# Kernel tuning notes

Measured on AMD Instinct MI355X. Metric: run time of the kernel, lower is better.

The kernel has to match this reference:

```python
import jax, jax.numpy as jnp
import numpy as np

# constants from source: INTERNAL_DIM=768, NUM_MEMORY_NETWORKS=8, NUM_SUB_NETWORKS=2, NUM_LAYERS=2
T, B, D, M, S, L, H = 8, 32, 768, 8, 2, 2, 8
d = D // S  # 384, per-subnetwork hidden dim
EPS = 1e-5


def _ln(x, g, b):
    mu = x.mean(-1, keepdims=True)
    v = ((x - mu) ** 2).mean(-1, keepdims=True)
    return (x - mu) / jnp.sqrt(v + EPS) * g + b


def setup_inputs() -> dict:
    key = jax.random.key(0)
    ks = jax.random.split(key, 10)
    rn = lambda k, shape, s: jax.random.normal(k, shape, jnp.float32) * s
    return {
        'x': rn(ks[0], (T, B, D), 1.0),
        'mem0': rn(ks[1], (M, B, D), 0.02),
        'attn_in_w': rn(ks[2], (M, 3 * D, D), D ** -0.5),
        'attn_in_b': jnp.zeros((M, 3 * D), jnp.float32),
        'attn_out_w': rn(ks[3], (M, D, D), D ** -0.5),
        'attn_out_b': jnp.zeros((M, D), jnp.float32),
        'heb_w': rn(ks[4], (M, S, L, d, d), 0.01),
        'heb_rw': rn(ks[5], (M, S, L, d, d), 0.01),
        'alpha': jnp.full((M, S, L, d), 0.02, jnp.float32),
        'decay': jnp.full((M, S, L, d), 0.005, jnp.float32),
        'ln_act_g': jnp.ones((M, S, L, d), jnp.float32),
        'ln_act_b': jnp.zeros((M, S, L, d), jnp.float32),
        'ln_rec_g': jnp.ones((M, S, L, d), jnp.float32),
        'ln_rec_b': jnp.zeros((M, S, L, d), jnp.float32),
        'pred_w1': rn(ks[6], (M, S, L, d, d), d ** -0.5),
        'pred_b1': jnp.zeros((M, S, L, d), jnp.float32),
        'pred_w2': rn(ks[7], (M, S, L, d, 3 * d), d ** -0.5),
        'pred_b2': jnp.zeros((M, S, L, 3 * d), jnp.float32),
        'out_w': rn(ks[8], (M, D, D), D ** -0.5),
        'out_b': jnp.zeros((M, D), jnp.float32),
        'ln_out_g': jnp.ones((M, D), jnp.float32),
        'ln_out_b': jnp.zeros((M, D), jnp.float32),
    }


def _mha(q, kv, in_w, in_b, out_w, out_b):
    # torch nn.MultiheadAttention: q [B,D], kv [Mkv,B,D] (seq-first)
    wq, wk, wv = in_w[:D], in_w[D:2 * D], in_w[2 * D:]
    bq, bk, bv = in_b[:D], in_b[D:2 * D], in_b[2 * D:]
    hd = D // H
    qh = (q @ wq.T + bq).reshape(B, H, hd) * hd ** -0.5
    kh = (kv @ wk.T + bk).reshape(-1, B, H, hd)
    vh = (kv @ wv.T + bv).reshape(-1, B, H, hd)
    a = jax.nn.softmax(jnp.einsum('bhd,sbhd->bhs', qh, kh), axis=-1)
    o = jnp.einsum('bhs,sbhd->bhd', a, vh).reshape(B, D)
    return o @ out_w.T + out_b


def _heb(xin, pa, pr, dp, sr, gb, W, Wr, W0, Wr0, al, dc, lag, lab, lrg, lrb, w1, b1, w2, b2):
    # one HebbianLayer step; xin/pa/pr/... [B,d], W/Wr [d,d]
    sg = jax.lax.stop_gradient
    # update_neuromodulators (previous neuromodulator state is detached in torch)
    nt = (jax.nn.relu(pa @ w1 + b1) @ w2 + b2).reshape(B, d, 3)
    pd, ps, pg = nt[..., 0], nt[..., 1], nt[..., 2]
    inv = 1.0 / jnp.maximum(ps, 1e-6)  # clamp(min=1e-6)
    dp = jnp.tanh(dp + pd * inv)
    sr = jax.nn.sigmoid(sr + ps)
    gb = jax.nn.sigmoid(gb + pg * inv)
    # hebbian_update: torch writes via .data.copy_ -> fully non-differentiable
    mod = al[None] * dp * sr  # [B,d] modulated alpha

    def upd(prev, Wm):
        a_sm = jax.nn.softmax(prev, axis=1)
        w_sm = jax.nn.softmax(Wm, axis=1)
        # mean_b a_sm[b,i] * mod[b,j] * w_sm[i,j]  (no [B,d,d] intermediate)
        return w_sm * (jnp.einsum('bi,bj->ij', a_sm, mod) / B)

    sd = dc * jax.nn.sigmoid(gb.mean(axis=0))  # scaled decay, diag
    W_new = sg(W + upd(pa, W) - sd[:, None] * W)
    Wr_new = sg(Wr + upd(pr, Wr) - sd[:, None] * Wr)
    # forward matmul uses the updated weight VALUE, gradient accumulates on leaf param
    W_eff = W_new + W0 - sg(W0)
    Wr_eff = Wr_new + Wr0 - sg(Wr0)
    rec = _ln(pa @ Wr_eff, lrg, lrb)
    act = _ln(jax.nn.relu(xin @ W_eff + rec), lag, lab)
    return act, (sg(act), sg(rec), sg(dp), sg(sr), sg(gb), W_new, Wr_new)


_heb_vm = jax.vmap(_heb)  # over P = M*S parallel subnetwork-layers


def reference(x, mem0, attn_in_w, attn_in_b, attn_out_w, attn_out_b, heb_w, heb_rw,
              alpha, decay, ln_act_g, ln_act_b, ln_rec_g, ln_rec_b,
              pred_w1, pred_b1, pred_w2, pred_b2, out_w, out_b, ln_out_g, ln_out_b):
    P = M * S
    rs = lambda a: a.reshape((P, L) + a.shape[3:])
    hw, hrw = rs(heb_w), rs(heb_rw)
    al, dc = rs(alpha), rs(decay)
    lag, lab, lrg, lrb = rs(ln_act_g), rs(ln_act_b), rs(ln_rec_g), rs(ln_rec_b)
    w1, b1, w2, b2 = rs(pred_w1), rs(pred_b1), rs(pred_w2), rs(pred_b2)
    z = jnp.zeros((P, L, B, d), x.dtype)
    carry0 = (mem0, z, z, z, z, z, hw, hrw)

    def step(carry, x_t):
        mem, pa, pr, dp, sr, gb, Wst, Wrst = carry
        # attention message passing: each memory network attends over all memories
        attn = jax.vmap(_mha, in_axes=(None, None, 0, 0, 0, 0))(
            x_t, mem, attn_in_w, attn_in_b, attn_out_w, attn_out_b)  # [M,B,D]
        # split into subnetworks: chunk i = u[:, i*d:(i+1)*d]
        h = attn.reshape(M, B, S, d).transpose(0, 2, 1, 3).reshape(P, B, d)
        new_st = []
        for l in range(L):
            h, st = _heb_vm(h, pa[:, l], pr[:, l], dp[:, l], sr[:, l], gb[:, l],
                            Wst[:, l], Wrst[:, l], hw[:, l], hrw[:, l],
                            al[:, l], dc[:, l], lag[:, l], lab[:, l], lrg[:, l], lrb[:, l],
                            w1[:, l], b1[:, l], w2[:, l], b2[:, l])
            new_st.append(st)
        stacked = tuple(jnp.stack([new_st[l][i] for l in range(L)], axis=1) for i in range(7))
        cat = h.reshape(M, S, B, d).transpose(0, 2, 1, 3).reshape(M, B, D)
        out = jnp.einsum('mbd,med->mbe', cat, out_w) + out_b[:, None]
        out = _ln(out, ln_out_g[:, None], ln_out_b[:, None])  # [M,B,D]
        return (out,) + stacked, out

    carry, _ = jax.lax.scan(step, carry0, x)
    return carry[0]  # final memory activations [M,B,D]
```

## Files before the change

kernel.cpp:

```cpp
#include <hip/hip_runtime.h>
#include <math.h>

namespace {

constexpr int T_ = 8, B_ = 32, D_ = 768, M_ = 8, S_ = 2, L_ = 2, H_ = 8;
constexpr int d_ = D_ / S_;
constexpr int P_ = M_ * S_;
constexpr int HD = D_ / H_;
constexpr float EPSF = 1e-5f;
constexpr int KNOFOLD = 1 << 30;

__device__ __forceinline__ float wredS(float v) {
#pragma unroll
  for (int o = 32; o; o >>= 1) v += __shfl_xor(v, o);
  return v;
}
__device__ __forceinline__ float wredM(float v) {
#pragma unroll
  for (int o = 32; o; o >>= 1) v = fmaxf(v, __shfl_xor(v, o));
  return v;
}
__device__ __forceinline__ float blockSum(float v, float* red, int nw) {
  v = wredS(v);
  if ((threadIdx.x & 63) == 0) red[threadIdx.x >> 6] = v;
  __syncthreads();
  float r = 0.f;
  for (int i = 0; i < nw; ++i) r += red[i];
  __syncthreads();
  return r;
}
__device__ __forceinline__ float blockMax(float v, float* red, int nw) {
  v = wredM(v);
  if ((threadIdx.x & 63) == 0) red[threadIdx.x >> 6] = v;
  __syncthreads();
  float r = red[0];
  for (int i = 1; i < nw; ++i) r = fmaxf(r, red[i]);
  __syncthreads();
  return r;
}
__device__ __forceinline__ float sigm(float x) { return 1.f / (1.f + expf(-x)); }

template <bool TRANSB, int EPI>
__device__ __forceinline__ void gemm_body(
    const float* __restrict__ Ab, int lda, const float* __restrict__ Wb,
    const float* __restrict__ biasz, float* __restrict__ Cb, int r0, int n0,
    int N, int K, float scale, int kfold, int kfoldOff) {
  __shared__ float As[32][36];
  __shared__ float Bs[32][132];
  const int tid = threadIdx.x;
  const int rg = tid >> 4, cg = tid & 15;
  float acc[2][8];
#pragma unroll
  for (int i = 0; i < 2; ++i)
#pragma unroll
    for (int j = 0; j < 8; ++j) acc[i][j] = 0.f;
  for (int k0 = 0; k0 < K; k0 += 32) {
    const float* Ak = Ab + (k0 >= kfold ? kfoldOff : 0);
    const int k0e = k0 - (k0 >= kfold ? kfold : 0);
    {
      const int r = tid >> 3, kq = (tid & 7) << 2;
      const float4 v = *(const float4*)(Ak + (size_t)(r0 + r) * lda + k0e + kq);
      As[kq + 0][r] = v.x; As[kq + 1][r] = v.y;
      As[kq + 2][r] = v.z; As[kq + 3][r] = v.w;
    }
#pragma unroll
    for (int i = 0; i < 4; ++i) {
      const int li = tid + i * 256;
      if (TRANSB) {
        const int n = li >> 3, kq = (li & 7) << 2;
        const float4 v = *(const float4*)(Wb + (size_t)(n0 + n) * K + k0 + kq);
        Bs[kq + 0][n] = v.x; Bs[kq + 1][n] = v.y;
        Bs[kq + 2][n] = v.z; Bs[kq + 3][n] = v.w;
      } else {
        const int k = li >> 5, nq = (li & 31) << 2;
        const float4 v = *(const float4*)(Wb + (size_t)(k0 + k) * N + n0 + nq);
        *(float4*)&Bs[k][nq] = v;
      }
    }
    __syncthreads();
#pragma unroll
    for (int kk = 0; kk < 32; ++kk) {
      const float2 a = *(const float2*)&As[kk][rg * 2];
      const float4 b0 = *(const float4*)&Bs[kk][cg * 4];
      const float4 b1 = *(const float4*)&Bs[kk][cg * 4 + 64];
      acc[0][0] += a.x * b0.x; acc[0][1] += a.x * b0.y;
      acc[0][2] += a.x * b0.z; acc[0][3] += a.x * b0.w;
      acc[0][4] += a.x * b1.x; acc[0][5] += a.x * b1.y;
      acc[0][6] += a.x * b1.z; acc[0][7] += a.x * b1.w;
      acc[1][0] += a.y * b0.x; acc[1][1] += a.y * b0.y;
      acc[1][2] += a.y * b0.z; acc[1][3] += a.y * b0.w;
      acc[1][4] += a.y * b1.x; acc[1][5] += a.y * b1.y;
      acc[1][6] += a.y * b1.z; acc[1][7] += a.y * b1.w;
    }
    __syncthreads();
  }
  float bv[8] = {0.f, 0.f, 0.f, 0.f, 0.f, 0.f, 0.f, 0.f};
  if (biasz) {
    const float* bb = biasz + n0 + cg * 4;
#pragma unroll
    for (int j = 0; j < 4; ++j) { bv[j] = bb[j]; bv[4 + j] = bb[64 + j]; }
  }
#pragma unroll
  for (int i = 0; i < 2; ++i) {
#pragma unroll
    for (int half = 0; half < 2; ++half) {
      float4 o;
      o.x = acc[i][half * 4 + 0] + bv[half * 4 + 0];
      o.y = acc[i][half * 4 + 1] + bv[half * 4 + 1];
      o.z = acc[i][half * 4 + 2] + bv[half * 4 + 2];
      o.w = acc[i][half * 4 + 3] + bv[half * 4 + 3];
      if (EPI == 1) {
        o.x = fmaxf(o.x, 0.f); o.y = fmaxf(o.y, 0.f);
        o.z = fmaxf(o.z, 0.f); o.w = fmaxf(o.w, 0.f);
      }
      if (EPI == 2) { o.x *= scale; o.y *= scale; o.z *= scale; o.w *= scale; }
      *(float4*)(Cb + (size_t)(r0 + rg * 2 + i) * N + n0 + half * 64 + cg * 4) = o;
    }
  }
}

template <bool TRANSB, int EPI>
__global__ __launch_bounds__(256) void k_gemm(
    const float* __restrict__ A, int sAhi, int sAlo, int lda,
    const float* __restrict__ W, int sW, const float* __restrict__ bias, int sB,
    float* __restrict__ C, int sC, int N, int K, float scale, int kfold,
    int kfoldOff) {
  const int z = blockIdx.z;
  const float* Ab = A + (size_t)(z >> 1) * sAhi + (size_t)(z & 1) * sAlo;
  const float* Wb = W + (size_t)z * sW;
  const float* biasz = bias ? bias + (size_t)z * sB : nullptr;
  float* Cb = C + (size_t)z * sC;
  gemm_body<TRANSB, EPI>(Ab, lda, Wb, biasz, Cb, blockIdx.y * 32,
                         blockIdx.x * 128, N, K, scale, kfold, kfoldOff);
}

__global__ __launch_bounds__(256) void k_recact(
    const float* __restrict__ A0, int hi0, int lo0, int lda0,
    const float* __restrict__ W0,
    const float* __restrict__ A1, int hi1, int lo1, int lda1,
    const float* __restrict__ W1, int sW, float* __restrict__ C0,
    float* __restrict__ C1) {
  const int z = blockIdx.z;
  const int which = z >> 4, zz = z & 15;
  const float* Ab = which ? A1 + (size_t)(zz >> 1) * hi1 + (size_t)(zz & 1) * lo1
                          : A0 + (size_t)(zz >> 1) * hi0 + (size_t)(zz & 1) * lo0;
  const int lda = which ? lda1 : lda0;
  const float* Wb = (which ? W1 : W0) + (size_t)zz * sW;
  float* Cb = (which ? C1 : C0) + (size_t)zz * (B_ * d_);
  gemm_body<false, 0>(Ab, lda, Wb, nullptr, Cb, 0, blockIdx.x * 128, d_, d_,
                      1.f, KNOFOLD, 0);
}

__global__ __launch_bounds__(64) void k_attn(const float* __restrict__ qb,
    const float* __restrict__ kvb, float* __restrict__ ob) {
  __shared__ float as_[8][8];
  const int mb = blockIdx.x, m = mb >> 5, b = mb & 31;
  const int t = threadIdx.x, h = t >> 3, s = t & 7;
  const float* qrow = qb + (size_t)mb * D_ + h * HD;
  const float* krow = kvb + ((size_t)m * 256 + s * 32 + b) * (2 * D_) + h * HD;
  float sc = 0.f;
#pragma unroll 8
  for (int e = 0; e < HD; ++e) sc += qrow[e] * krow[e];
  float mx = sc;
#pragma unroll
  for (int o = 1; o < 8; o <<= 1) mx = fmaxf(mx, __shfl_xor(mx, o));
  const float ex = expf(sc - mx);
  float sm = ex;
#pragma unroll
  for (int o = 1; o < 8; o <<= 1) sm += __shfl_xor(sm, o);
  as_[h][s] = ex / sm;
  __syncthreads();
  const float* vbase = kvb + (size_t)m * 256 * (2 * D_) + D_;
  for (int e = t; e < D_; e += 64) {
    const int hh = e / HD;
    float o = 0.f;
#pragma unroll
    for (int ss = 0; ss < 8; ++ss)
      o += as_[hh][ss] * vbase[(size_t)(ss * 32 + b) * (2 * D_) + e];
    ob[(size_t)mb * D_ + e] = o;
  }
}

__global__ __launch_bounds__(384) void k_mod(const float* __restrict__ nt,
    float* __restrict__ dp, float* __restrict__ sr, float* __restrict__ gb,
    float* __restrict__ mod, float* __restrict__ sd,
    const float* __restrict__ alpha, const float* __restrict__ decay, int l) {
  const int p = blockIdx.x, j = threadIdx.x;
  const int pl = p * L_ + l;
  const float al = alpha[(size_t)pl * d_ + j];
  const float dc = decay[(size_t)pl * d_ + j];
  const size_t sbase = (size_t)pl * B_ * d_;
  float gsum = 0.f;
  for (int b = 0; b < B_; ++b) {
    const float* row = nt + ((size_t)p * B_ + b) * (3 * d_) + 3 * j;
    const float pd = row[0], ps = row[1], pg = row[2];
    const float inv = 1.f / fmaxf(ps, 1e-6f);
    const size_t ix = sbase + (size_t)b * d_ + j;
    const float dpv = tanhf(dp[ix] + pd * inv);
    const float srv = sigm(sr[ix] + ps);
    const float gbv = sigm(gb[ix] + pg * inv);
    dp[ix] = dpv; sr[ix] = srv; gb[ix] = gbv;
    mod[((size_t)p * B_ + b) * d_ + j] = al * dpv * srv;
    gsum += gbv;
  }
  sd[(size_t)p * d_ + j] = dc * sigm(gsum * (1.f / B_));
}

__global__ __launch_bounds__(256) void k_wsm(float* __restrict__ Wst,
    float* __restrict__ Wrst, const float* __restrict__ pa,
    const float* __restrict__ pr, const float* __restrict__ mod,
    const float* __restrict__ sd, int l) {
  __shared__ float mods[B_][d_];
  __shared__ float asms[8][B_];
  __shared__ float rm_s[B_], rs_s[B_];
  __shared__ float red[4];
  const int i0 = blockIdx.x * 8, p = blockIdx.y, which = blockIdx.z;
  const int tid = threadIdx.x;
  const int pl = p * L_ + l;
  float* W = (which ? Wrst : Wst) + (size_t)pl * d_ * d_;
  const float* act = (which ? pr : pa) + (size_t)pl * B_ * d_;
  for (int ix = tid; ix < B_ * d_; ix += 256)
    mods[ix / d_][ix % d_] = mod[(size_t)p * B_ * d_ + ix];
  {
    const int bb = tid >> 3, l8 = tid & 7;
    const float* ar = act + (size_t)bb * d_;
    float mx = -3.4e38f;
    for (int j = l8; j < d_; j += 8) mx = fmaxf(mx, ar[j]);
#pragma unroll
    for (int o = 1; o < 8; o <<= 1) mx = fmaxf(mx, __shfl_xor(mx, o));
    float s = 0.f;
    for (int j = l8; j < d_; j += 8) s += expf(ar[j] - mx);
#pragma unroll
    for (int o = 1; o < 8; o <<= 1) s += __shfl_xor(s, o);
    if (l8 == 0) { rm_s[bb] = mx; rs_s[bb] = s; }
  }
  __syncthreads();
  {
    const int ii = tid >> 5, b = tid & 31;
    asms[ii][b] = expf(act[(size_t)b * d_ + i0 + ii] - rm_s[b]) / rs_s[b];
  }
  __syncthreads();
  for (int ii = 0; ii < 8; ++ii) {
    const int i = i0 + ii;
    float* Wrow = W + (size_t)i * d_;
    const float w1v = Wrow[tid];
    const bool a2 = tid < (d_ - 256);
    const float w2v = a2 ? Wrow[tid + 256] : 0.f;
    const float mx = blockMax(a2 ? fmaxf(w1v, w2v) : w1v, red, 4);
    const float e1 = expf(w1v - mx);
    const float e2 = a2 ? expf(w2v - mx) : 0.f;
    const float ssum = blockSum(e1 + e2, red, 4);
    const float sdi = sd[(size_t)p * d_ + i];
    float o1 = 0.f, o2 = 0.f;
    const float* am = asms[ii];
#pragma unroll 8
    for (int b = 0; b < B_; ++b) {
      const float a = am[b];
      o1 += a * mods[b][tid];
      if (a2) o2 += a * mods[b][tid + 256];
    }
    Wrow[tid] = w1v * (1.f - sdi) + (e1 / ssum) * (o1 * (1.f / B_));
    if (a2) Wrow[tid + 256] = w2v * (1.f - sdi) + (e2 / ssum) * (o2 * (1.f / B_));
    __syncthreads();
  }
}

__global__ __launch_bounds__(128) void k_lnpair(const float* __restrict__ gr,
    const float* __restrict__ ga, float* __restrict__ prs,
    float* __restrict__ pas, const float* __restrict__ lrg,
    const float* __restrict__ lrb, const float* __restrict__ lag,
    const float* __restrict__ lab, int l) {
  __shared__ float red[2];
  const int pb = blockIdx.x, p = pb >> 5, b = pb & 31;
  const int pl = p * L_ + l;
  const int t = threadIdx.x;
  const size_t soff = ((size_t)pl * B_ + b) * d_;
  const float* xr = gr + (size_t)pb * d_;
  float v0 = xr[t], v1 = xr[t + 128], v2 = xr[t + 256];
  float mu = blockSum(v0 + v1 + v2, red, 2) * (1.f / d_);
  float e0 = v0 - mu, e1 = v1 - mu, e2 = v2 - mu;
  float va = blockSum(e0 * e0 + e1 * e1 + e2 * e2, red, 2) * (1.f / d_);
  float inv = 1.f / sqrtf(va + EPSF);
  const float* G = lrg + (size_t)pl * d_;
  const float* Bv = lrb + (size_t)pl * d_;
  const float r0v = e0 * inv * G[t] + Bv[t];
  const float r1v = e1 * inv * G[t + 128] + Bv[t + 128];
  const float r2v = e2 * inv * G[t + 256] + Bv[t + 256];
  prs[soff + t] = r0v;
  prs[soff + t + 128] = r1v;
  prs[soff + t + 256] = r2v;
  const float* xa = ga + (size_t)pb * d_;
  float a0 = fmaxf(xa[t] + r0v, 0.f);
  float a1 = fmaxf(xa[t + 128] + r1v, 0.f);
  float a2 = fmaxf(xa[t + 256] + r2v, 0.f);
  mu = blockSum(a0 + a1 + a2, red, 2) * (1.f / d_);
  e0 = a0 - mu; e1 = a1 - mu; e2 = a2 - mu;
  va = blockSum(e0 * e0 + e1 * e1 + e2 * e2, red, 2) * (1.f / d_);
  inv = 1.f / sqrtf(va + EPSF);
  const float* G2 = lag + (size_t)pl * d_;
  const float* B2 = lab + (size_t)pl * d_;
  pas[soff + t] = e0 * inv * G2[t] + B2[t];
  pas[soff + t + 128] = e1 * inv * G2[t + 128] + B2[t + 128];
  pas[soff + t + 256] = e2 * inv * G2[t + 256] + B2[t + 256];
}

__global__ __launch_bounds__(256) void k_lnout(const float* __restrict__ pre,
    float* __restrict__ memo, const float* __restrict__ gg,
    const float* __restrict__ bb) {
  __shared__ float red[4];
  const int mb = blockIdx.x, m = mb >> 5;
  const float* x = pre + (size_t)mb * D_;
  const int t = threadIdx.x;
  const float v0 = x[t], v1 = x[t + 256], v2 = x[t + 512];
  const float mu = blockSum(v0 + v1 + v2, red, 4) * (1.f / D_);
  const float e0 = v0 - mu, e1 = v1 - mu, e2 = v2 - mu;
  const float va = blockSum(e0 * e0 + e1 * e1 + e2 * e2, red, 4) * (1.f / D_);
  const float inv = 1.f / sqrtf(va + EPSF);
  const float* G = gg + (size_t)m * D_;
  const float* Bv = bb + (size_t)m * D_;
  float* o = memo + (size_t)mb * D_;
  o[t] = e0 * inv * G[t] + Bv[t];
  o[t + 256] = e1 * inv * G[t + 256] + Bv[t + 256];
  o[t + 512] = e2 * inv * G[t + 512] + Bv[t + 512];
}

}

extern "C" void kernel_launch(void* const* d_in, const int* in_sizes, int n_in,
                              void* d_out, int out_size, void* d_ws, size_t ws_size,
                              hipStream_t stream) {
  const float* x     = (const float*)d_in[0];
  const float* mem0  = (const float*)d_in[1];
  const float* ainw  = (const float*)d_in[2];
  const float* ainb  = (const float*)d_in[3];
  const float* aoutw = (const float*)d_in[4];
  const float* aoutb = (const float*)d_in[5];
  const float* hebw  = (const float*)d_in[6];
  const float* hebrw = (const float*)d_in[7];
  const float* alpha = (const float*)d_in[8];
  const float* decay = (const float*)d_in[9];
  const float* lag   = (const float*)d_in[10];
  const float* lab   = (const float*)d_in[11];
  const float* lrg   = (const float*)d_in[12];
  const float* lrb   = (const float*)d_in[13];
  const float* pw1   = (const float*)d_in[14];
  const float* pb1   = (const float*)d_in[15];
  const float* pw2   = (const float*)d_in[16];
  const float* pb2   = (const float*)d_in[17];
  const float* outw  = (const float*)d_in[18];
  const float* outb  = (const float*)d_in[19];
  const float* lng   = (const float*)d_in[20];
  const float* lnb   = (const float*)d_in[21];

  float* w = (float*)d_ws;
  size_t off = 0;
  auto alloc = [&](size_t n) { float* p = w + off; off += n; return p; };
  float* mem   = alloc((size_t)M_ * B_ * D_);
  float* qb    = alloc((size_t)M_ * B_ * D_);
  float* kvb   = alloc((size_t)M_ * M_ * B_ * 2 * D_);
  float* ob    = alloc((size_t)M_ * B_ * D_);
  float* attnh = alloc((size_t)M_ * B_ * D_);
  float* t1    = alloc((size_t)P_ * B_ * d_);
  float* nt    = alloc((size_t)P_ * B_ * 3 * d_);
  float* modb  = alloc((size_t)P_ * B_ * d_);
  float* sdb   = alloc((size_t)P_ * d_);
  float* gtmp  = alloc((size_t)2 * P_ * B_ * d_);
  float* otmp  = alloc((size_t)M_ * B_ * D_);
  float* pa    = alloc((size_t)P_ * L_ * B_ * d_);
  float* pr    = alloc((size_t)P_ * L_ * B_ * d_);
  float* dp    = alloc((size_t)P_ * L_ * B_ * d_);
  float* sr    = alloc((size_t)P_ * L_ * B_ * d_);
  float* gbst  = alloc((size_t)P_ * L_ * B_ * d_);
  float* Wst   = alloc((size_t)P_ * L_ * d_ * d_);
  float* Wrst  = alloc((size_t)P_ * L_ * d_ * d_);
  float* gtmp0 = gtmp;
  float* gtmp1 = gtmp + (size_t)P_ * B_ * d_;
  (void)in_sizes; (void)n_in; (void)out_size; (void)ws_size;

  hipMemcpyAsync(mem, mem0, sizeof(float) * M_ * B_ * D_, hipMemcpyDeviceToDevice, stream);
  hipMemcpyAsync(Wst, hebw, sizeof(float) * P_ * L_ * d_ * d_, hipMemcpyDeviceToDevice, stream);
  hipMemcpyAsync(Wrst, hebrw, sizeof(float) * P_ * L_ * d_ * d_, hipMemcpyDeviceToDevice, stream);
  hipMemsetAsync(pa, 0, sizeof(float) * 5 * P_ * L_ * B_ * d_, stream);

  const float qscale = 1.0f / sqrtf((float)HD);
  const int LBd = L_ * B_ * d_;
  const int Bd = B_ * d_;

  auto gemm = [&](bool transB, int epi, const float* A, int sAhi, int sAlo,
                  int lda, const float* Wp, int sW, const float* bias, int sB,
                  float* C, int sC, int R, int N, int K, int G, float scale,
                  int kfold, int kfoldOff) {
    dim3 grid(N / 128, R / 32, G), blk(256);
    if (transB && epi == 0)
      k_gemm<true, 0><<<grid, blk, 0, stream>>>(A, sAhi, sAlo, lda, Wp, sW, bias, sB, C, sC, N, K, scale, kfold, kfoldOff);
    else if (transB && epi == 2)
      k_gemm<true, 2><<<grid, blk, 0, stream>>>(A, sAhi, sAlo, lda, Wp, sW, bias, sB, C, sC, N, K, scale, kfold, kfoldOff);
    else if (!transB && epi == 0)
      k_gemm<false, 0><<<grid, blk, 0, stream>>>(A, sAhi, sAlo, lda, Wp, sW, bias, sB, C, sC, N, K, scale, kfold, kfoldOff);
    else
      k_gemm<false, 1><<<grid, blk, 0, stream>>>(A, sAhi, sAlo, lda, Wp, sW, bias, sB, C, sC, N, K, scale, kfold, kfoldOff);
  };

  for (int t = 0; t < T_; ++t) {
    const float* xt = x + (size_t)t * B_ * D_;
    gemm(true, 2, xt, 0, 0, D_, ainw, 3 * D_ * D_, ainb, 3 * D_, qb, B_ * D_,
         B_, D_, D_, M_, qscale, KNOFOLD, 0);
    gemm(true, 0, mem, 0, 0, D_, ainw + D_ * D_, 3 * D_ * D_, ainb + D_, 3 * D_,
         kvb, M_ * B_ * 2 * D_, M_ * B_, 2 * D_, D_, M_, 1.f, KNOFOLD, 0);
    k_attn<<<dim3(M_ * B_), dim3(64), 0, stream>>>(qb, kvb, ob);
    gemm(true, 0, ob, 2 * B_ * D_, B_ * D_, D_, aoutw, D_ * D_, aoutb, D_,
         attnh, B_ * D_, B_, D_, D_, M_, 1.f, KNOFOLD, 0);

    for (int l = 0; l < L_; ++l) {
      gemm(false, 1, pa + (size_t)l * Bd, 2 * LBd, LBd, d_,
           pw1 + (size_t)l * d_ * d_, L_ * d_ * d_, pb1 + l * d_, L_ * d_,
           t1, Bd, B_, d_, d_, P_, 1.f, KNOFOLD, 0);
      gemm(false, 0, t1, 2 * Bd, Bd, d_, pw2 + (size_t)l * d_ * 3 * d_,
           L_ * d_ * 3 * d_, pb2 + l * 3 * d_, L_ * 3 * d_, nt, 3 * Bd,
           B_, 3 * d_, d_, P_, 1.f, KNOFOLD, 0);
      k_mod<<<dim3(P_), dim3(d_), 0, stream>>>(nt, dp, sr, gbst, modb, sdb,
                                               alpha, decay, l);
      k_wsm<<<dim3(d_ / 8, P_, 2), dim3(256), 0, stream>>>(Wst, Wrst, pa, pr,
                                                           modb, sdb, l);
      if (l == 0)
        k_recact<<<dim3(3, 1, 32), dim3(256), 0, stream>>>(
            pa + (size_t)l * Bd, 2 * LBd, LBd, d_, Wrst + (size_t)l * d_ * d_,
            attnh, B_ * D_, d_, D_, Wst + (size_t)l * d_ * d_,
            L_ * d_ * d_, gtmp0, gtmp1);
      else
        k_recact<<<dim3(3, 1, 32), dim3(256), 0, stream>>>(
            pa + (size_t)l * Bd, 2 * LBd, LBd, d_, Wrst + (size_t)l * d_ * d_,
            pa, 2 * LBd, LBd, d_, Wst + (size_t)l * d_ * d_,
            L_ * d_ * d_, gtmp0, gtmp1);
      k_lnpair<<<dim3(P_ * B_), dim3(128), 0, stream>>>(gtmp0, gtmp1, pr, pa,
                                                        lrg, lrb, lag, lab, l);
    }

    gemm(true, 0, pa + Bd, 8 * Bd, 4 * Bd, d_, outw, D_ * D_, outb, D_,
         otmp, B_ * D_, B_, D_, D_, M_, 1.f, d_, 2 * Bd);
    k_lnout<<<dim3(M_ * B_), dim3(256), 0, stream>>>(otmp, mem, lng, lnb);
  }

  hipMemcpyAsync(d_out, mem, sizeof(float) * M_ * B_ * D_, hipMemcpyDeviceToDevice, stream);
}
```

Baseline: 5.248 ms.

## Prefetch GEMM tiles, fuse QKV launches, hoist softmax stats, warp-level W softmax

Several changes land together. The GEMM body now prefetches the next K-tile into registers while the current tile is being computed, and the Q and KV projection GEMMs are merged into one launch. The per-row activation softmax max and sum move into k_mod, so k_wsm no longer recomputes them in every block. k_wsm now gives each wavefront one weight row, replacing block-wide reductions and barriers with warp shuffles, and each block covers 32 rows instead of 8. The cost is more registers for the prefetched tiles, extra LDS for the asme tile, and some extra serial work in k_mod.

```diff
diff --git a/kernel.cpp b/kernel.cpp
--- a/kernel.cpp
+++ b/kernel.cpp
@@ -13,11 +13,6 @@
 __device__ __forceinline__ float wredS(float v) {
 #pragma unroll
   for (int o = 32; o; o >>= 1) v += __shfl_xor(v, o);
-  return v;
-}
-__device__ __forceinline__ float wredM(float v) {
-#pragma unroll
-  for (int o = 32; o; o >>= 1) v = fmaxf(v, __shfl_xor(v, o));
   return v;
 }
 __device__ __forceinline__ float blockSum(float v, float* red, int nw) {
@@ -29,60 +24,72 @@
   __syncthreads();
   return r;
 }
-__device__ __forceinline__ float blockMax(float v, float* red, int nw) {
-  v = wredM(v);
-  if ((threadIdx.x & 63) == 0) red[threadIdx.x >> 6] = v;
-  __syncthreads();
-  float r = red[0];
-  for (int i = 1; i < nw; ++i) r = fmaxf(r, red[i]);
-  __syncthreads();
-  return r;
-}
 __device__ __forceinline__ float sigm(float x) { return 1.f / (1.f + expf(-x)); }
 
+struct SmemGemm {
+  float As[32][34];
+  float Bs[32][132];
+};
+
 template <bool TRANSB, int EPI>
-__device__ __forceinline__ void gemm_body(
+__device__ __forceinline__ void gemm_body(SmemGemm& sm,
     const float* __restrict__ Ab, int lda, const float* __restrict__ Wb,
     const float* __restrict__ biasz, float* __restrict__ Cb, int r0, int n0,
     int N, int K, float scale, int kfold, int kfoldOff) {
-  __shared__ float As[32][36];
-  __shared__ float Bs[32][132];
   const int tid = threadIdx.x;
   const int rg = tid >> 4, cg = tid & 15;
-  float acc[2][8];
-#pragma unroll
-  for (int i = 0; i < 2; ++i)
-#pragma unroll
-    for (int j = 0; j < 8; ++j) acc[i][j] = 0.f;
-  for (int k0 = 0; k0 < K; k0 += 32) {
+  const int ar = tid >> 3, akq = (tid & 7) << 2;
+  float4 pA;
+  float4 pB[4];
+  auto loadA = [&](int k0) {
     const float* Ak = Ab + (k0 >= kfold ? kfoldOff : 0);
     const int k0e = k0 - (k0 >= kfold ? kfold : 0);
-    {
-      const int r = tid >> 3, kq = (tid & 7) << 2;
-      const float4 v = *(const float4*)(Ak + (size_t)(r0 + r) * lda + k0e + kq);
-      As[kq + 0][r] = v.x; As[kq + 1][r] = v.y;
-      As[kq + 2][r] = v.z; As[kq + 3][r] = v.w;
-    }
+    pA = *(const float4*)(Ak + (size_t)(r0 + ar) * lda + k0e + akq);
+  };
+  auto loadB = [&](int k0) {
 #pragma unroll
     for (int i = 0; i < 4; ++i) {
       const int li = tid + i * 256;
       if (TRANSB) {
         const int n = li >> 3, kq = (li & 7) << 2;
-        const float4 v = *(const float4*)(Wb + (size_t)(n0 + n) * K + k0 + kq);
-        Bs[kq + 0][n] = v.x; Bs[kq + 1][n] = v.y;
-        Bs[kq + 2][n] = v.z; Bs[kq + 3][n] = v.w;
+        pB[i] = *(const float4*)(Wb + (size_t)(n0 + n) * K + k0 + kq);
       } else {
         const int k = li >> 5, nq = (li & 31) << 2;
-        const float4 v = *(const float4*)(Wb + (size_t)(k0 + k) * N + n0 + nq);
-        *(float4*)&Bs[k][nq] = v;
+        pB[i] = *(const float4*)(Wb + (size_t)(k0 + k) * N + n0 + nq);
       }
     }
+  };
+  auto storeLDS = [&]() {
+    sm.As[akq + 0][ar] = pA.x; sm.As[akq + 1][ar] = pA.y;
+    sm.As[akq + 2][ar] = pA.z; sm.As[akq + 3][ar] = pA.w;
+#pragma unroll
+    for (int i = 0; i < 4; ++i) {
+      const int li = tid + i * 256;
+      if (TRANSB) {
+        const int n = li >> 3, kq = (li & 7) << 2;
+        sm.Bs[kq + 0][n] = pB[i].x; sm.Bs[kq + 1][n] = pB[i].y;
+        sm.Bs[kq + 2][n] = pB[i].z; sm.Bs[kq + 3][n] = pB[i].w;
+      } else {
+        const int k = li >> 5, nq = (li & 31) << 2;
+        *(float4*)&sm.Bs[k][nq] = pB[i];
+      }
+    }
+  };
+  float acc[2][8];
+#pragma unroll
+  for (int i = 0; i < 2; ++i)
+#pragma unroll
+    for (int j = 0; j < 8; ++j) acc[i][j] = 0.f;
+  loadA(0); loadB(0);
+  for (int k0 = 0; k0 < K; k0 += 32) {
+    storeLDS();
     __syncthreads();
+    if (k0 + 32 < K) { loadA(k0 + 32); loadB(k0 + 32); }
 #pragma unroll
     for (int kk = 0; kk < 32; ++kk) {
-      const float2 a = *(const float2*)&As[kk][rg * 2];
-      const float4 b0 = *(const float4*)&Bs[kk][cg * 4];
-      const float4 b1 = *(const float4*)&Bs[kk][cg * 4 + 64];
+      const float2 a = *(const float2*)&sm.As[kk][rg * 2];
+      const float4 b0 = *(const float4*)&sm.Bs[kk][cg * 4];
+      const float4 b1 = *(const float4*)&sm.Bs[kk][cg * 4 + 64];
       acc[0][0] += a.x * b0.x; acc[0][1] += a.x * b0.y;
       acc[0][2] += a.x * b0.z; acc[0][3] += a.x * b0.w;
       acc[0][4] += a.x * b1.x; acc[0][5] += a.x * b1.y;
@@ -125,13 +132,33 @@
     const float* __restrict__ W, int sW, const float* __restrict__ bias, int sB,
     float* __restrict__ C, int sC, int N, int K, float scale, int kfold,
     int kfoldOff) {
+  __shared__ SmemGemm sm;
   const int z = blockIdx.z;
   const float* Ab = A + (size_t)(z >> 1) * sAhi + (size_t)(z & 1) * sAlo;
   const float* Wb = W + (size_t)z * sW;
   const float* biasz = bias ? bias + (size_t)z * sB : nullptr;
   float* Cb = C + (size_t)z * sC;
-  gemm_body<TRANSB, EPI>(Ab, lda, Wb, biasz, Cb, blockIdx.y * 32,
+  gemm_body<TRANSB, EPI>(sm, Ab, lda, Wb, biasz, Cb, blockIdx.y * 32,
                          blockIdx.x * 128, N, K, scale, kfold, kfoldOff);
+}
+
+__global__ __launch_bounds__(256) void k_qkv(
+    const float* __restrict__ xt, const float* __restrict__ mem,
+    const float* __restrict__ ainw, const float* __restrict__ ainb,
+    float* __restrict__ qb, float* __restrict__ kvb, float qscale) {
+  __shared__ SmemGemm sm;
+  const int z = blockIdx.z;
+  const float* Wz = ainw + (size_t)z * 3 * D_ * D_;
+  const float* bz = ainb + (size_t)z * 3 * D_;
+  if (blockIdx.y == 8) {
+    if (blockIdx.x >= 6) return;
+    gemm_body<true, 2>(sm, xt, D_, Wz, bz, qb + (size_t)z * B_ * D_, 0,
+                       blockIdx.x * 128, D_, D_, qscale, KNOFOLD, 0);
+  } else {
+    gemm_body<true, 0>(sm, mem, D_, Wz + D_ * D_, bz + D_,
+                       kvb + (size_t)z * M_ * B_ * 2 * D_, blockIdx.y * 32,
+                       blockIdx.x * 128, 2 * D_, D_, 1.f, KNOFOLD, 0);
+  }
 }
 
 __global__ __launch_bounds__(256) void k_recact(
@@ -140,6 +167,7 @@
     const float* __restrict__ A1, int hi1, int lo1, int lda1,
     const float* __restrict__ W1, int sW, float* __restrict__ C0,
     float* __restrict__ C1) {
+  __shared__ SmemGemm sm;
   const int z = blockIdx.z;
   const int which = z >> 4, zz = z & 15;
   const float* Ab = which ? A1 + (size_t)(zz >> 1) * hi1 + (size_t)(zz & 1) * lo1
@@ -147,7 +175,7 @@
   const int lda = which ? lda1 : lda0;
   const float* Wb = (which ? W1 : W0) + (size_t)zz * sW;
   float* Cb = (which ? C1 : C0) + (size_t)zz * (B_ * d_);
-  gemm_body<false, 0>(Ab, lda, Wb, nullptr, Cb, 0, blockIdx.x * 128, d_, d_,
+  gemm_body<false, 0>(sm, Ab, lda, Wb, nullptr, Cb, 0, blockIdx.x * 128, d_, d_,
                       1.f, KNOFOLD, 0);
 }
 
@@ -184,7 +212,9 @@
 __global__ __launch_bounds__(384) void k_mod(const float* __restrict__ nt,
     float* __restrict__ dp, float* __restrict__ sr, float* __restrict__ gb,
     float* __restrict__ mod, float* __restrict__ sd,
-    const float* __restrict__ alpha, const float* __restrict__ decay, int l) {
+    const float* __restrict__ alpha, const float* __restrict__ decay,
+    const float* __restrict__ pa, const float* __restrict__ pr,
+    float* __restrict__ rmax, float* __restrict__ rsum, int l) {
   const int p = blockIdx.x, j = threadIdx.x;
   const int pl = p * L_ + l;
   const float al = alpha[(size_t)pl * d_ + j];
@@ -204,64 +234,79 @@
     gsum += gbv;
   }
   sd[(size_t)p * d_ + j] = dc * sigm(gsum * (1.f / B_));
+  const int g = j >> 3, l8 = j & 7;
+  for (int rr = g; rr < 64; rr += 48) {
+    const int which = rr >> 5, b = rr & 31;
+    const float* src = (which ? pr : pa) + (sbase + (size_t)b * d_);
+    float mx = -3.4e38f;
+    for (int jj = l8; jj < d_; jj += 8) mx = fmaxf(mx, src[jj]);
+#pragma unroll
+    for (int o = 1; o < 8; o <<= 1) mx = fmaxf(mx, __shfl_xor(mx, o));
+    float s = 0.f;
+    for (int jj = l8; jj < d_; jj += 8) s += expf(src[jj] - mx);
+#pragma unroll
+    for (int o = 1; o < 8; o <<= 1) s += __shfl_xor(s, o);
+    if (l8 == 0) {
+      rmax[which * (P_ * B_) + p * B_ + b] = mx;
+      rsum[which * (P_ * B_) + p * B_ + b] = s;
+    }
+  }
 }
 
 __global__ __launch_bounds__(256) void k_wsm(float* __restrict__ Wst,
     float* __restrict__ Wrst, const float* __restrict__ pa,
     const float* __restrict__ pr, const float* __restrict__ mod,
-    const float* __restrict__ sd, int l) {
+    const float* __restrict__ sd, const float* __restrict__ rmax,
+    const float* __restrict__ rsum, int l) {
   __shared__ float mods[B_][d_];
-  __shared__ float asms[8][B_];
-  __shared__ float rm_s[B_], rs_s[B_];
-  __shared__ float red[4];
-  const int i0 = blockIdx.x * 8, p = blockIdx.y, which = blockIdx.z;
+  __shared__ float asme[32][32];
+  const int i0 = blockIdx.x * 32, p = blockIdx.y, which = blockIdx.z;
   const int tid = threadIdx.x;
   const int pl = p * L_ + l;
   float* W = (which ? Wrst : Wst) + (size_t)pl * d_ * d_;
   const float* act = (which ? pr : pa) + (size_t)pl * B_ * d_;
+  const float* rm = rmax + which * (P_ * B_) + p * B_;
+  const float* rs = rsum + which * (P_ * B_) + p * B_;
   for (int ix = tid; ix < B_ * d_; ix += 256)
     mods[ix / d_][ix % d_] = mod[(size_t)p * B_ * d_ + ix];
-  {
-    const int bb = tid >> 3, l8 = tid & 7;
-    const float* ar = act + (size_t)bb * d_;
-    float mx = -3.4e38f;
-    for (int j = l8; j < d_; j += 8) mx = fmaxf(mx, ar[j]);
-#pragma unroll
-    for (int o = 1; o < 8; o <<= 1) mx = fmaxf(mx, __shfl_xor(mx, o));
-    float s = 0.f;
-    for (int j = l8; j < d_; j += 8) s += expf(ar[j] - mx);
-#pragma unroll
-    for (int o = 1; o < 8; o <<= 1) s += __shfl_xor(s, o);
-    if (l8 == 0) { rm_s[bb] = mx; rs_s[bb] = s; }
+#pragma unroll
+  for (int q = 0; q < 4; ++q) {
+    const int idx = tid + q * 256;
+    const int ii = idx >> 5, b = idx & 31;
+    asme[ii][b] = expf(act[(size_t)b * d_ + i0 + ii] - rm[b]) / rs[b];
   }
   __syncthreads();
-  {
-    const int ii = tid >> 5, b = tid & 31;
-    asms[ii][b] = expf(act[(size_t)b * d_ + i0 + ii] - rm_s[b]) / rs_s[b];
-  }
-  __syncthreads();
-  for (int ii = 0; ii < 8; ++ii) {
+  const int w = tid >> 6, lane = tid & 63;
+  for (int it = 0; it < 8; ++it) {
+    const int ii = it * 4 + w;
     const int i = i0 + ii;
     float* Wrow = W + (size_t)i * d_;
-    const float w1v = Wrow[tid];
-    const bool a2 = tid < (d_ - 256);
-    const float w2v = a2 ? Wrow[tid + 256] : 0.f;
-    const float mx = blockMax(a2 ? fmaxf(w1v, w2v) : w1v, red, 4);
-    const float e1 = expf(w1v - mx);
-    const float e2 = a2 ? expf(w2v - mx) : 0.f;
-    const float ssum = blockSum(e1 + e2, red, 4);
+    float wv[6], ev[6];
+    float mx = -3.4e38f;
+#pragma unroll
+    for (int e = 0; e < 6; ++e) {
+      wv[e] = Wrow[lane + 64 * e];
+      mx = fmaxf(mx, wv[e]);
+    }
+#pragma unroll
+    for (int o = 1; o < 64; o <<= 1) mx = fmaxf(mx, __shfl_xor(mx, o));
+    float s = 0.f;
+#pragma unroll
+    for (int e = 0; e < 6; ++e) { ev[e] = expf(wv[e] - mx); s += ev[e]; }
+#pragma unroll
+    for (int o = 1; o < 64; o <<= 1) s += __shfl_xor(s, o);
     const float sdi = sd[(size_t)p * d_ + i];
-    float o1 = 0.f, o2 = 0.f;
-    const float* am = asms[ii];
-#pragma unroll 8
+    float o6[6] = {0.f, 0.f, 0.f, 0.f, 0.f, 0.f};
     for (int b = 0; b < B_; ++b) {
-      const float a = am[b];
-      o1 += a * mods[b][tid];
-      if (a2) o2 += a * mods[b][tid + 256];
-    }
-    Wrow[tid] = w1v * (1.f - sdi) + (e1 / ssum) * (o1 * (1.f / B_));
-    if (a2) Wrow[tid + 256] = w2v * (1.f - sdi) + (e2 / ssum) * (o2 * (1.f / B_));
-    __syncthreads();
+      const float a = asme[ii][b];
+#pragma unroll
+      for (int e = 0; e < 6; ++e) o6[e] += a * mods[b][lane + 64 * e];
+    }
+    const float rinv = 1.f / s;
+#pragma unroll
+    for (int e = 0; e < 6; ++e)
+      Wrow[lane + 64 * e] =
+          wv[e] * (1.f - sdi) + ev[e] * rinv * (o6[e] * (1.f / B_));
   }
 }
 
@@ -364,6 +409,8 @@
   float* nt    = alloc((size_t)P_ * B_ * 3 * d_);
   float* modb  = alloc((size_t)P_ * B_ * d_);
   float* sdb   = alloc((size_t)P_ * d_);
+  float* rmaxb = alloc(2 * P_ * B_);
+  float* rsumb = alloc(2 * P_ * B_);
   float* gtmp  = alloc((size_t)2 * P_ * B_ * d_);
   float* otmp  = alloc((size_t)M_ * B_ * D_);
   float* pa    = alloc((size_t)P_ * L_ * B_ * d_);
@@ -403,10 +450,8 @@
 
   for (int t = 0; t < T_; ++t) {
     const float* xt = x + (size_t)t * B_ * D_;
-    gemm(true, 2, xt, 0, 0, D_, ainw, 3 * D_ * D_, ainb, 3 * D_, qb, B_ * D_,
-         B_, D_, D_, M_, qscale, KNOFOLD, 0);
-    gemm(true, 0, mem, 0, 0, D_, ainw + D_ * D_, 3 * D_ * D_, ainb + D_, 3 * D_,
-         kvb, M_ * B_ * 2 * D_, M_ * B_, 2 * D_, D_, M_, 1.f, KNOFOLD, 0);
+    k_qkv<<<dim3(12, 9, M_), dim3(256), 0, stream>>>(xt, mem, ainw, ainb, qb,
+                                                     kvb, qscale);
     k_attn<<<dim3(M_ * B_), dim3(64), 0, stream>>>(qb, kvb, ob);
     gemm(true, 0, ob, 2 * B_ * D_, B_ * D_, D_, aoutw, D_ * D_, aoutb, D_,
          attnh, B_ * D_, B_, D_, D_, M_, 1.f, KNOFOLD, 0);
@@ -419,9 +464,10 @@
            L_ * d_ * 3 * d_, pb2 + l * 3 * d_, L_ * 3 * d_, nt, 3 * Bd,
            B_, 3 * d_, d_, P_, 1.f, KNOFOLD, 0);
       k_mod<<<dim3(P_), dim3(d_), 0, stream>>>(nt, dp, sr, gbst, modb, sdb,
-                                               alpha, decay, l);
-      k_wsm<<<dim3(d_ / 8, P_, 2), dim3(256), 0, stream>>>(Wst, Wrst, pa, pr,
-                                                           modb, sdb, l);
+                                               alpha, decay, pa, pr, rmaxb,
+                                               rsumb, l);
+      k_wsm<<<dim3(d_ / 32, P_, 2), dim3(256), 0, stream>>>(
+          Wst, Wrst, pa, pr, modb, sdb, rmaxb, rsumb, l);
       if (l == 0)
         k_recact<<<dim3(3, 1, 32), dim3(256), 0, stream>>>(
             pa + (size_t)l * Bd, 2 * LBd, LBd, d_, Wrst + (size_t)l * d_ * d_,
```

New measurement: 6.753 ms. 28.7% more time.
